# Performance work log

Hardware: AMD Instinct MI355X
Metric: run time of the kernel (lower is better)

The kernel has to match this reference:

```python
import jax, jax.numpy as jnp
import numpy as np

N, E, D_IN, H, Z = 50000, 800000, 256, 96, 32
NEG_SLOPE = 0.2  # PyG GATConv default
BN_EPS = 1e-5


def _gat(x, src, dst, W, a, b, n):
    """Single-head GATConv (PyG semantics, self-loops already in src/dst)."""
    h = x @ W                                   # [N, F']
    e = jax.nn.leaky_relu((h @ a[0])[src] + (h @ a[1])[dst], NEG_SLOPE)  # [E]
    m = jax.ops.segment_max(e, dst, num_segments=n)
    ex = jnp.exp(e - m[dst])
    s = jax.ops.segment_sum(ex, dst, num_segments=n)
    alpha = ex / s[dst]                         # softmax over incoming edges
    out = jax.ops.segment_sum(alpha[:, None] * h[src], dst, num_segments=n)
    return out + b


def _bn(x, g, b):
    # BatchNorm1d in training mode: biased batch stats over nodes
    mu = jnp.mean(x, axis=0)
    v = jnp.var(x, axis=0)
    return g * (x - mu) / jnp.sqrt(v + BN_EPS) + b


def setup_inputs() -> dict:
    key = jax.random.key(0)
    ks = jax.random.split(key, 32)
    inp = {}
    inp["x"] = jax.random.normal(ks[0], (N, D_IN), jnp.float32)
    inp["edge_index"] = jax.random.randint(ks[1], (2, E), 0, N)
    inp["eps"] = jax.random.normal(ks[2], (N, Z), jnp.float32)

    def xav(k, di, do):
        s = float(np.sqrt(2.0 / (di + do)))
        return jax.random.normal(k, (di, do), jnp.float32) * s

    layers = [("enc1", D_IN, H), ("enc2", H, H), ("mu", H, Z), ("lv", H, Z),
              ("dec1", Z, H), ("dec2", H, H), ("out", H, D_IN)]
    ki = 3
    for nm, di, do in layers:
        inp[nm + "_W"] = xav(ks[ki], di, do)
        inp[nm + "_a"] = jax.random.normal(ks[ki + 1], (2, do), jnp.float32) * 0.1
        inp[nm + "_b"] = jnp.zeros((do,), jnp.float32)
        ki += 2
    for nm in ["bne1", "bne2", "bnd1", "bnd2"]:
        inp[nm + "_g"] = jnp.ones((H,), jnp.float32)
        inp[nm + "_b"] = jnp.zeros((H,), jnp.float32)
    return inp


def reference(x, edge_index, eps,
              enc1_W, enc1_a, enc1_b, enc2_W, enc2_a, enc2_b,
              mu_W, mu_a, mu_b, lv_W, lv_a, lv_b,
              dec1_W, dec1_a, dec1_b, dec2_W, dec2_a, dec2_b,
              out_W, out_a, out_b,
              bne1_g, bne1_b, bne2_g, bne2_b, bnd1_g, bnd1_b, bnd2_g, bnd2_b):
    n = x.shape[0]
    loop = jnp.arange(n)
    src = jnp.concatenate([edge_index[0], loop])  # add self-loops (GAT default)
    dst = jnp.concatenate([edge_index[1], loop])

    # ---- GraphEncoder ----
    h0 = jax.nn.relu(_bn(_gat(x, src, dst, enc1_W, enc1_a, enc1_b, n), bne1_g, bne1_b))
    h1 = jax.nn.relu(_bn(_gat(h0, src, dst, enc2_W, enc2_a, enc2_b, n), bne2_g, bne2_b))
    h = h1 + h0  # residual from layer 0
    q_m = _gat(h, src, dst, mu_W, mu_a, mu_b, n)
    q_s = _gat(h, src, dst, lv_W, lv_a, lv_b, n)
    std = jax.nn.softplus(q_s) + 1e-6
    q_z = q_m + std * eps  # rsample

    # ---- GraphDecoder ----
    d0 = jax.nn.relu(_bn(_gat(q_z, src, dst, dec1_W, dec1_a, dec1_b, n), bnd1_g, bnd1_b))
    d1 = jax.nn.relu(_bn(_gat(d0, src, dst, dec2_W, dec2_a, dec2_b, n), bnd2_g, bnd2_b))
    d = d1 + d0
    recon = jax.nn.softmax(_gat(d, src, dst, out_W, out_a, out_b, n), axis=-1)
    return q_z, q_m, q_s, recon
```

## Files before the change

### kernel.cpp

```cpp
#include <hip/hip_runtime.h>
#include <math.h>

#define NN 50000
#define EE 800000
#define HDIM 96
#define ZDIM 32
#define MAXD 64
#define NBUK 64
#define BCAP 16384
#define BMUL 1341
#define NBB 512
#define MGRID 782
#define CDIV(a,b) (((a)+(b)-1)/(b))

typedef unsigned int uint;
typedef unsigned short ushort;
typedef __bf16 bf16x8 __attribute__((ext_vector_type(8)));
typedef float f32x4 __attribute__((ext_vector_type(4)));

__device__ __forceinline__ ushort f2b(float f) {
  uint x = __float_as_uint(f);
  return (ushort)((x + 0x7fffu + ((x >> 16) & 1u)) >> 16);
}
__device__ __forceinline__ uint pack2(float a, float b) {
  return (uint)f2b(a) | ((uint)f2b(b) << 16);
}
__device__ __forceinline__ float blo(uint u) { return __uint_as_float(u << 16); }
__device__ __forceinline__ float bhi(uint u) { return __uint_as_float(u & 0xffff0000u); }
__device__ __forceinline__ float lrelu(float v) { return v > 0.f ? v : 0.2f * v; }

__device__ __forceinline__ void red_scsh(const float* __restrict__ sb,
                                         const float* __restrict__ g,
                                         const float* __restrict__ b,
                                         float* s_c, float* s_h, int tid) {
  if (tid < 96) {
    float su = 0.f, sq = 0.f;
#pragma unroll 8
    for (int j = 0; j < NBUK; j++) {
      su += sb[j * 192 + tid];
      sq += sb[j * 192 + 96 + tid];
    }
    float mu = su * (1.0f / NN);
    float va = sq * (1.0f / NN) - mu * mu;
    float sc = g[tid] * rsqrtf(va + 1e-5f);
    s_c[tid] = sc;
    s_h[tid] = fmaf(-sc, mu, b[tid]);
  }
}

struct PrepArgs { const float* W[7]; const float* a[7]; };

__global__ void k_prep(PrepArgs p, ushort* __restrict__ wt, float* __restrict__ avb,
                       int* __restrict__ zbase, int zcount) {
  const int SDin[6]  = {256, 96, 96, 32, 96, 96};
  const int SDout[6] = {96, 96, 64, 96, 96, 256};
  const int SL[6]    = {0, 1, 2, 4, 5, 6};
  const int SWoff[6] = {0, 24576, 33792, 39936, 43008, 52224};
  int y = blockIdx.y;
  if (y < 6) {
    int Din = SDin[y], Dout = SDout[y];
    int n = Din * Dout;
    ushort* wo = wt + SWoff[y];
    if (y == 2) {
      const float* W2 = p.W[2];
      const float* W3 = p.W[3];
      for (int o = blockIdx.x * 256 + threadIdx.x; o < n; o += 96 * 256) {
        int c = o / Din, k = o % Din;
        float w = (c < 32) ? W2[(size_t)k * 32 + c] : W3[(size_t)k * 32 + (c - 32)];
        wo[o] = f2b(w);
      }
    } else {
      const float* W = p.W[SL[y]];
      for (int o = blockIdx.x * 256 + threadIdx.x; o < n; o += 96 * 256) {
        int c = o / Din, k = o % Din;
        wo[o] = f2b(W[(size_t)k * Dout + c]);
      }
    }
  } else if (y == 6) {
    int wave = (blockIdx.x * 256 + threadIdx.x) >> 6;
    int lane = threadIdx.x & 63;
    for (int row = wave; row < 128; row += 96 * 4) {
      int l = (row < 32) ? 4 : 6;
      int k = (row < 32) ? row : row - 32;
      int Dout = (l == 4) ? 96 : 256;
      const float* W = p.W[l];
      const float* a = p.a[l];
      float s0 = 0.f, s1 = 0.f;
      for (int c = lane; c < Dout; c += 64) {
        float w = W[(size_t)k * Dout + c];
        s0 = fmaf(w, a[c], s0);
        s1 = fmaf(w, a[Dout + c], s1);
      }
      for (int o = 32; o > 0; o >>= 1) {
        s0 += __shfl_down(s0, o);
        s1 += __shfl_down(s1, o);
      }
      if (lane == 0) {
        if (l == 4) { avb[k] = s0; avb[32 + k] = s1; }
        else { avb[64 + k] = s0; avb[160 + k] = s1; }
      }
    }
  } else {
    for (int i = blockIdx.x * 256 + threadIdx.x; i < zcount; i += 96 * 256)
      zbase[i] = 0;
  }
}

__global__ __launch_bounds__(256) void k_partA(const int* __restrict__ eidx,
                                               int* __restrict__ bcnt,
                                               uint* __restrict__ barr) {
  __shared__ int hist[NBUK];
  __shared__ int hbase[NBUK];
  const int tot = EE + NN;
  const int tid = threadIdx.x;
  int base = blockIdx.x * 512 + tid;
  if (tid < NBUK) hist[tid] = 0;
  __syncthreads();
  int dv[2], sv[2], bk[2], ofs[2];
  bool ok[2];
#pragma unroll
  for (int j = 0; j < 2; j++) {
    int e = base + j * 256;
    ok[j] = e < tot;
    dv[j] = sv[j] = bk[j] = ofs[j] = 0;
    if (ok[j]) {
      if (e < EE) { sv[j] = eidx[e]; dv[j] = eidx[EE + e]; }
      else { sv[j] = dv[j] = e - EE; }
      bk[j] = (dv[j] * BMUL) >> 20;
      ofs[j] = atomicAdd(&hist[bk[j]], 1);
    }
  }
  __syncthreads();
  if (tid < NBUK) hbase[tid] = atomicAdd(&bcnt[tid], hist[tid]);
  __syncthreads();
#pragma unroll
  for (int j = 0; j < 2; j++) {
    if (ok[j]) {
      int w = hbase[bk[j]] + ofs[j];
      if (w < BCAP) barr[bk[j] * BCAP + w] = ((uint)dv[j] << 16) | (uint)sv[j];
    }
  }
}

template<int DIN, int DOUT, int AMODE, bool BF16_OUT, bool ADD_BIAS, int EPI, bool STATS>
__device__ __forceinline__ void mfma_body(
    int bid, const void* __restrict__ A1, const void* __restrict__ A2,
    const float* __restrict__ sbA, const float* __restrict__ gA, const float* __restrict__ bA,
    const float* __restrict__ sbB, const float* __restrict__ gB, const float* __restrict__ bB,
    const ushort* __restrict__ Wt, const float* __restrict__ bias,
    void* __restrict__ outp, const float* __restrict__ aA, const float* __restrict__ aB,
    float* __restrict__ el, float* __restrict__ er,
    float2* __restrict__ elp, float2* __restrict__ erp, float* __restrict__ sbout) {
  constexpr int NT = DOUT / 16;
  constexpr int KS = DIN / 32;
  const int tid = threadIdx.x;
  const int lane = tid & 63;
  const int wv = tid >> 6;
  const int row0 = bid * 64 + wv * 16;
  const int cl = lane & 15;
  const int g = lane >> 4;
  const int arow = min(row0 + cl, NN - 1);
  __shared__ float s_c1[96], s_h1[96], s_c2[96], s_h2[96];
  if constexpr (AMODE >= 2) {
    red_scsh(sbA, gA, bA, s_c1, s_h1, tid);
    if constexpr (AMODE == 3) red_scsh(sbB, gB, bB, s_c2, s_h2, tid);
    __syncthreads();
  }
  f32x4 acc[NT];
#pragma unroll
  for (int t = 0; t < NT; t++) acc[t] = (f32x4){0.f, 0.f, 0.f, 0.f};
#pragma unroll
  for (int ks = 0; ks < KS; ks++) {
    bf16x8 af;
    if constexpr (AMODE == 0) {
      af = *(const bf16x8*)((const ushort*)A1 + (size_t)arow * DIN + ks * 32 + g * 8);
    } else if constexpr (AMODE == 1) {
      const float* Af = (const float*)A1 + (size_t)arow * DIN + ks * 32 + g * 8;
      float4 lo = *(const float4*)Af;
      float4 hi = *(const float4*)(Af + 4);
      union { uint4 u; bf16x8 v; } cvt;
      cvt.u.x = pack2(lo.x, lo.y); cvt.u.y = pack2(lo.z, lo.w);
      cvt.u.z = pack2(hi.x, hi.y); cvt.u.w = pack2(hi.z, hi.w);
      af = cvt.v;
    } else {
      const float* p1 = (const float*)A1 + (size_t)arow * DIN + ks * 32 + g * 8;
      const float* p2 = (const float*)A2 + (size_t)arow * DIN + ks * 32 + g * 8;
      const int f0 = ks * 32 + g * 8;
      float v[8];
#pragma unroll
      for (int j = 0; j < 8; j++) {
        float t = fmaxf(fmaf(s_c1[f0 + j], p1[j], s_h1[f0 + j]), 0.f);
        if constexpr (AMODE == 3)
          t += fmaxf(fmaf(s_c2[f0 + j], p2[j], s_h2[f0 + j]), 0.f);
        v[j] = t;
      }
      union { uint4 u; bf16x8 b8; } cv;
      cv.u.x = pack2(v[0], v[1]); cv.u.y = pack2(v[2], v[3]);
      cv.u.z = pack2(v[4], v[5]); cv.u.w = pack2(v[6], v[7]);
      af = cv.b8;
    }
#pragma unroll
    for (int t = 0; t < NT; t++) {
      bf16x8 bf = *(const bf16x8*)(Wt + (size_t)(t * 16 + cl) * DIN + ks * 32 + g * 8);
      acc[t] = __builtin_amdgcn_mfma_f32_16x16x32_bf16(af, bf, acc[t], 0, 0, 0);
    }
  }
  if constexpr (EPI == 1) {
#pragma unroll
    for (int r = 0; r < 4; r++) {
      float l0 = 0.f, l1 = 0.f;
#pragma unroll
      for (int t = 0; t < NT; t++) {
        float w0 = aA[t * 16 + cl], w1 = aA[DOUT + t * 16 + cl];
        l0 = fmaf(acc[t][r], w0, l0);
        l1 = fmaf(acc[t][r], w1, l1);
      }
#pragma unroll
      for (int m = 1; m < 16; m <<= 1) {
        l0 += __shfl_xor(l0, m);
        l1 += __shfl_xor(l1, m);
      }
      int row = row0 + g * 4 + r;
      if (cl == 0 && row < NN) { el[row] = l0; er[row] = l1; }
    }
  }
  if constexpr (EPI == 2) {
#pragma unroll
    for (int r = 0; r < 4; r++) {
      float m0 = 0.f, m1 = 0.f, v0 = 0.f, v1 = 0.f;
#pragma unroll
      for (int t = 0; t < 2; t++) {
        int c = t * 16 + cl;
        m0 = fmaf(acc[t][r], aA[c], m0);
        m1 = fmaf(acc[t][r], aA[32 + c], m1);
        v0 = fmaf(acc[t + 2][r], aB[c], v0);
        v1 = fmaf(acc[t + 2][r], aB[32 + c], v1);
      }
#pragma unroll
      for (int m = 1; m < 16; m <<= 1) {
        m0 += __shfl_xor(m0, m); m1 += __shfl_xor(m1, m);
        v0 += __shfl_xor(v0, m); v1 += __shfl_xor(v1, m);
      }
      int row = row0 + g * 4 + r;
      if (cl == 0 && row < NN) {
        elp[row] = make_float2(m0, v0);
        erp[row] = make_float2(m1, v1);
      }
    }
  }
  if constexpr (ADD_BIAS) {
#pragma unroll
    for (int t = 0; t < NT; t++) {
      float bv = bias[t * 16 + cl];
#pragma unroll
      for (int r = 0; r < 4; r++) acc[t][r] += bv;
    }
  }
  if constexpr (STATS) {
    __shared__ float s_su[96], s_sq[96];
    if (tid < 96) { s_su[tid] = 0.f; s_sq[tid] = 0.f; }
    __syncthreads();
#pragma unroll
    for (int t = 0; t < NT; t++) {
      float su = 0.f, sq = 0.f;
#pragma unroll
      for (int r = 0; r < 4; r++) {
        if (row0 + g * 4 + r < NN) {
          float v = acc[t][r];
          su += v;
          sq = fmaf(v, v, sq);
        }
      }
      atomicAdd(&s_su[t * 16 + cl], su);
      atomicAdd(&s_sq[t * 16 + cl], sq);
    }
    __syncthreads();
    if (tid < 96) {
      float* bk = sbout + (bid & 63) * 192;
      atomicAdd(&bk[tid], s_su[tid]);
      atomicAdd(&bk[96 + tid], s_sq[tid]);
    }
  }
  if constexpr (EPI == 3) {
    float mx[4], sm[4];
#pragma unroll
    for (int r = 0; r < 4; r++) mx[r] = -3.4e38f;
#pragma unroll
    for (int t = 0; t < NT; t++)
#pragma unroll
      for (int r = 0; r < 4; r++) mx[r] = fmaxf(mx[r], acc[t][r]);
#pragma unroll
    for (int r = 0; r < 4; r++) {
#pragma unroll
      for (int msk = 1; msk < 16; msk <<= 1)
        mx[r] = fmaxf(mx[r], __shfl_xor(mx[r], msk));
      sm[r] = 0.f;
    }
#pragma unroll
    for (int t = 0; t < NT; t++)
#pragma unroll
      for (int r = 0; r < 4; r++) { acc[t][r] = expf(acc[t][r] - mx[r]); sm[r] += acc[t][r]; }
#pragma unroll
    for (int r = 0; r < 4; r++) {
#pragma unroll
      for (int msk = 1; msk < 16; msk <<= 1) sm[r] += __shfl_xor(sm[r], msk);
      sm[r] = 1.f / sm[r];
    }
#pragma unroll
    for (int t = 0; t < NT; t++)
#pragma unroll
      for (int r = 0; r < 4; r++) acc[t][r] *= sm[r];
  }
#pragma unroll
  for (int r = 0; r < 4; r++) {
    int grow = row0 + g * 4 + r;
    if (grow >= NN) continue;
    if constexpr (BF16_OUT) {
      ushort* o = (ushort*)outp + (size_t)grow * DOUT + cl;
#pragma unroll
      for (int t = 0; t < NT; t++) o[t * 16] = f2b(acc[t][r]);
    } else {
      float* o = (float*)outp + (size_t)grow * DOUT + cl;
#pragma unroll
      for (int t = 0; t < NT; t++) o[t * 16] = acc[t][r];
    }
  }
}

template<int DIN, int DOUT, int AMODE, bool BF16_OUT, bool ADD_BIAS, int EPI, bool STATS>
__global__ __launch_bounds__(256) void k_mfma(
    const void* __restrict__ A1, const void* __restrict__ A2,
    const float* __restrict__ sbA, const float* __restrict__ gA, const float* __restrict__ bA,
    const float* __restrict__ sbB, const float* __restrict__ gB, const float* __restrict__ bB,
    const ushort* __restrict__ Wt, const float* __restrict__ bias,
    void* __restrict__ outp, const float* __restrict__ aA, const float* __restrict__ aB,
    float* __restrict__ el, float* __restrict__ er,
    float2* __restrict__ elp, float2* __restrict__ erp, float* __restrict__ sbout) {
  mfma_body<DIN, DOUT, AMODE, BF16_OUT, ADD_BIAS, EPI, STATS>(
      blockIdx.x, A1, A2, sbA, gA, bA, sbB, gB, bB, Wt, bias, outp, aA, aB,
      el, er, elp, erp, sbout);
}

__global__ __launch_bounds__(256) void k_fatB(
    const int* __restrict__ bcnt, const uint* __restrict__ barr,
    int* __restrict__ dcnt, ushort* __restrict__ srcs,
    const float* __restrict__ x, const ushort* __restrict__ Wt,
    ushort* __restrict__ hbf, const float* __restrict__ aA,
    float* __restrict__ el, float* __restrict__ er) {
  if (blockIdx.x < NBB) {
    const int bucket = blockIdx.x & 63;
    const int j = blockIdx.x >> 6;
    const int n = min(bcnt[bucket], BCAP);
    const uint* bp = barr + bucket * BCAP;
    for (int idx = j * 256 + (int)threadIdx.x; idx < n; idx += 2048) {
      uint e = bp[idx];
      int d = (int)(e >> 16);
      int s = (int)(e & 0xffffu);
      int p = atomicAdd(&dcnt[d], 1);
      if (p < MAXD) srcs[d * MAXD + p] = (ushort)s;
    }
  } else {
    mfma_body<256, 96, 1, true, false, 1, false>(
        blockIdx.x - NBB, x, nullptr, nullptr, nullptr, nullptr, nullptr, nullptr, nullptr,
        Wt, nullptr, hbf, aA, nullptr, el, er, nullptr, nullptr, nullptr);
  }
}

template<int D, bool BF16O, bool STATS>
__global__ __launch_bounds__(256) void k_agg1(
    const ushort* __restrict__ hb, const float* __restrict__ el,
    const float* __restrict__ er, const int* __restrict__ dcnt,
    const ushort* __restrict__ srcs, const float* __restrict__ bias,
    void* __restrict__ out, float* __restrict__ sbuck) {
  constexpr int LPN = (D <= 32) ? 32 : 64;
  constexpr int NPB = 256 / LPN;
  constexpr int NU = D / 2;
  const int tid = threadIdx.x;
  const int slot = tid / LPN;
  const int ln = tid % LPN;
  const int i = blockIdx.x * NPB + slot;
  const int beg = i * MAXD;
  const int deg = min(dcnt[i], MAXD);
  const int end = beg + deg;
  const float eri = er[i];
  const uint* h32 = (const uint*)hb;
  __shared__ float s_al[256];
  __shared__ uint s_of[256];
  float v0 = -3.4e38f;
  int sv0 = 0;
  if (ln < deg) { sv0 = srcs[beg + ln]; v0 = lrelu(el[sv0] + eri); }
  float m = v0;
  for (int c = beg + LPN; c < end; c += LPN) {
    int e = c + ln;
    if (e < end) m = fmaxf(m, lrelu(el[srcs[e]] + eri));
  }
  for (int o = LPN / 2; o; o >>= 1) m = fmaxf(m, __shfl_xor(m, o, LPN));
  float s = (ln < deg) ? expf(v0 - m) : 0.f;
  for (int c = beg + LPN; c < end; c += LPN) {
    int e = c + ln;
    if (e < end) s += expf(lrelu(el[srcs[e]] + eri) - m);
  }
  for (int o = LPN / 2; o; o >>= 1) s += __shfl_xor(s, o, LPN);
  const float inv = 1.0f / s;
  float acc0 = 0.f, acc1 = 0.f;
  if (ln < deg) { s_al[tid] = expf(v0 - m) * inv; s_of[tid] = (uint)sv0 * NU; }
  const int base = slot * LPN;
  int nv = min(LPN, deg);
  if (ln < NU) {
    int t = 0;
    for (; t + 8 <= nv; t += 8) {
      uint o0 = s_of[base + t],     o1 = s_of[base + t + 1];
      uint o2 = s_of[base + t + 2], o3 = s_of[base + t + 3];
      uint o4 = s_of[base + t + 4], o5 = s_of[base + t + 5];
      uint o6 = s_of[base + t + 6], o7 = s_of[base + t + 7];
      uint u0 = h32[o0 + ln], u1 = h32[o1 + ln], u2 = h32[o2 + ln], u3 = h32[o3 + ln];
      uint u4 = h32[o4 + ln], u5 = h32[o5 + ln], u6 = h32[o6 + ln], u7 = h32[o7 + ln];
      float a0 = s_al[base + t],     a1 = s_al[base + t + 1];
      float a2 = s_al[base + t + 2], a3 = s_al[base + t + 3];
      float a4 = s_al[base + t + 4], a5 = s_al[base + t + 5];
      float a6 = s_al[base + t + 6], a7 = s_al[base + t + 7];
      acc0 = fmaf(a0, blo(u0), acc0); acc1 = fmaf(a0, bhi(u0), acc1);
      acc0 = fmaf(a1, blo(u1), acc0); acc1 = fmaf(a1, bhi(u1), acc1);
      acc0 = fmaf(a2, blo(u2), acc0); acc1 = fmaf(a2, bhi(u2), acc1);
      acc0 = fmaf(a3, blo(u3), acc0); acc1 = fmaf(a3, bhi(u3), acc1);
      acc0 = fmaf(a4, blo(u4), acc0); acc1 = fmaf(a4, bhi(u4), acc1);
      acc0 = fmaf(a5, blo(u5), acc0); acc1 = fmaf(a5, bhi(u5), acc1);
      acc0 = fmaf(a6, blo(u6), acc0); acc1 = fmaf(a6, bhi(u6), acc1);
      acc0 = fmaf(a7, blo(u7), acc0); acc1 = fmaf(a7, bhi(u7), acc1);
    }
    for (; t + 4 <= nv; t += 4) {
      uint o0 = s_of[base + t],     o1 = s_of[base + t + 1];
      uint o2 = s_of[base + t + 2], o3 = s_of[base + t + 3];
      uint u0 = h32[o0 + ln], u1 = h32[o1 + ln], u2 = h32[o2 + ln], u3 = h32[o3 + ln];
      float a0 = s_al[base + t],     a1 = s_al[base + t + 1];
      float a2 = s_al[base + t + 2], a3 = s_al[base + t + 3];
      acc0 = fmaf(a0, blo(u0), acc0); acc1 = fmaf(a0, bhi(u0), acc1);
      acc0 = fmaf(a1, blo(u1), acc0); acc1 = fmaf(a1, bhi(u1), acc1);
      acc0 = fmaf(a2, blo(u2), acc0); acc1 = fmaf(a2, bhi(u2), acc1);
      acc0 = fmaf(a3, blo(u3), acc0); acc1 = fmaf(a3, bhi(u3), acc1);
    }
    for (; t < nv; t++) {
      float a = s_al[base + t];
      uint u = h32[s_of[base + t] + ln];
      acc0 = fmaf(a, blo(u), acc0);
      acc1 = fmaf(a, bhi(u), acc1);
    }
  }
  for (int c = beg + LPN; c < end; c += LPN) {
    int e = c + ln;
    if (e < end) {
      int sv = srcs[e];
      s_al[tid] = expf(lrelu(el[sv] + eri) - m) * inv;
      s_of[tid] = (uint)sv * NU;
    }
    int nv2 = min(LPN, end - c);
    if (ln < NU) {
      for (int t = 0; t < nv2; t++) {
        float a = s_al[base + t];
        uint u = h32[s_of[base + t] + ln];
        acc0 = fmaf(a, blo(u), acc0);
        acc1 = fmaf(a, bhi(u), acc1);
      }
    }
  }
  float o0 = 0.f, o1 = 0.f;
  if (ln < NU) {
    float b0 = bias ? bias[2 * ln] : 0.f;
    float b1 = bias ? bias[2 * ln + 1] : 0.f;
    o0 = acc0 + b0;
    o1 = acc1 + b1;
    if constexpr (BF16O) {
      ((uint*)out)[(size_t)i * NU + ln] = pack2(o0, o1);
    } else {
      ((float2*)out)[(size_t)i * NU + ln] = make_float2(o0, o1);
    }
  }
  if constexpr (STATS) {
    __shared__ float s_val[4][96];
    if (ln < NU) {
      s_val[slot][2 * ln] = o0;
      s_val[slot][2 * ln + 1] = o1;
    }
    __syncthreads();
    if (tid < 96) {
      float su = 0.f, sq = 0.f;
#pragma unroll
      for (int s2 = 0; s2 < 4; s2++) {
        float v = s_val[s2][tid];
        su += v;
        sq = fmaf(v, v, sq);
      }
      float* bk = sbuck + (blockIdx.x & 63) * 192;
      atomicAdd(&bk[tid], su);
      atomicAdd(&bk[96 + tid], sq);
    }
  }
}

__global__ __launch_bounds__(256) void k_aggmulv(
    const ushort* __restrict__ hb, const float2* __restrict__ elp,
    const float2* __restrict__ erp, const int* __restrict__ dcnt,
    const ushort* __restrict__ srcs, const float* __restrict__ bmu,
    const float* __restrict__ blv, float* __restrict__ qm, float* __restrict__ qs,
    const float* __restrict__ eps, float* __restrict__ qz,
    ushort* __restrict__ qzbf, const float* __restrict__ av4,
    float* __restrict__ el, float* __restrict__ er) {
  const int tid = threadIdx.x;
  const int slot = tid >> 5;
  const int ln = tid & 31;
  const int i = blockIdx.x * 8 + slot;
  if (i >= NN) return;
  const int beg = i * MAXD;
  const int deg = min(dcnt[i], MAXD);
  const int end = beg + deg;
  const float2 eri = erp[i];
  const uint* h32 = (const uint*)hb;
  __shared__ float s_am[256];
  __shared__ float s_av[256];
  __shared__ uint s_of[256];
  float v0m = -3.4e38f, v0l = -3.4e38f;
  int sv0 = 0;
  if (ln < deg) {
    sv0 = srcs[beg + ln];
    float2 p = elp[sv0];
    v0m = lrelu(p.x + eri.x);
    v0l = lrelu(p.y + eri.y);
  }
  float mm = v0m, ml = v0l;
  for (int c = beg + 32; c < end; c += 32) {
    int e = c + ln;
    if (e < end) {
      float2 p = elp[srcs[e]];
      mm = fmaxf(mm, lrelu(p.x + eri.x));
      ml = fmaxf(ml, lrelu(p.y + eri.y));
    }
  }
  for (int o = 16; o; o >>= 1) {
    mm = fmaxf(mm, __shfl_xor(mm, o, 32));
    ml = fmaxf(ml, __shfl_xor(ml, o, 32));
  }
  float sm = 0.f, sl = 0.f;
  if (ln < deg) { sm = expf(v0m - mm); sl = expf(v0l - ml); }
  for (int c = beg + 32; c < end; c += 32) {
    int e = c + ln;
    if (e < end) {
      float2 p = elp[srcs[e]];
      sm += expf(lrelu(p.x + eri.x) - mm);
      sl += expf(lrelu(p.y + eri.y) - ml);
    }
  }
  for (int o = 16; o; o >>= 1) {
    sm += __shfl_xor(sm, o, 32);
    sl += __shfl_xor(sl, o, 32);
  }
  const float invm = 1.0f / sm, invl = 1.0f / sl;
  float acc0 = 0.f, acc1 = 0.f;
  if (ln < deg) {
    s_am[tid] = expf(v0m - mm) * invm;
    s_av[tid] = expf(v0l - ml) * invl;
    s_of[tid] = (uint)sv0 * 32;
  }
  const int base = slot * 32;
  const float* s_sel = (ln < 16) ? s_am : s_av;
  int nv = min(32, deg);
  int t = 0;
  for (; t + 4 <= nv; t += 4) {
    uint o0 = s_of[base + t],     o1 = s_of[base + t + 1];
    uint o2 = s_of[base + t + 2], o3 = s_of[base + t + 3];
    uint u0 = h32[o0 + ln], u1 = h32[o1 + ln], u2 = h32[o2 + ln], u3 = h32[o3 + ln];
    float a0 = s_sel[base + t],     a1 = s_sel[base + t + 1];
    float a2 = s_sel[base + t + 2], a3 = s_sel[base + t + 3];
    acc0 = fmaf(a0, blo(u0), acc0); acc1 = fmaf(a0, bhi(u0), acc1);
    acc0 = fmaf(a1, blo(u1), acc0); acc1 = fmaf(a1, bhi(u1), acc1);
    acc0 = fmaf(a2, blo(u2), acc0); acc1 = fmaf(a2, bhi(u2), acc1);
    acc0 = fmaf(a3, blo(u3), acc0); acc1 = fmaf(a3, bhi(u3), acc1);
  }
  for (; t < nv; t++) {
    float a = s_sel[base + t];
    uint u = h32[s_of[base + t] + ln];
    acc0 = fmaf(a, blo(u), acc0);
    acc1 = fmaf(a, bhi(u), acc1);
  }
  for (int c = beg + 32; c < end; c += 32) {
    int e = c + ln;
    if (e < end) {
      int sv = srcs[e];
      float2 p = elp[sv];
      s_am[tid] = expf(lrelu(p.x + eri.x) - mm) * invm;
      s_av[tid] = expf(lrelu(p.y + eri.y) - ml) * invl;
      s_of[tid] = (uint)sv * 32;
    }
    int nv2 = min(32, end - c);
    for (int tt = 0; tt < nv2; tt++) {
      float a = s_sel[base + tt];
      uint u = h32[s_of[base + tt] + ln];
      acc0 = fmaf(a, blo(u), acc0);
      acc1 = fmaf(a, bhi(u), acc1);
    }
  }
  float b0 = (ln < 16) ? bmu[2 * ln] : blv[2 * (ln - 16)];
  float b1 = (ln < 16) ? bmu[2 * ln + 1] : blv[2 * (ln - 16) + 1];
  float o0 = acc0 + b0, o1 = acc1 + b1;
  if (ln < 16) ((float2*)qm)[(size_t)i * 16 + ln] = make_float2(o0, o1);
  else ((float2*)qs)[(size_t)i * 16 + (ln - 16)] = make_float2(o0, o1);
  float q0 = __shfl_xor(o0, 16, 32);
  float q1 = __shfl_xor(o1, 16, 32);
  if (ln < 16) {
    float2 ep = ((const float2*)eps)[(size_t)i * 16 + ln];
    float sp0 = fmaxf(q0, 0.f) + log1pf(expf(-fabsf(q0))) + 1e-6f;
    float sp1 = fmaxf(q1, 0.f) + log1pf(expf(-fabsf(q1))) + 1e-6f;
    float z0 = fmaf(sp0, ep.x, o0);
    float z1 = fmaf(sp1, ep.y, o1);
    ((float2*)qz)[(size_t)i * 16 + ln] = make_float2(z0, z1);
    ((uint*)qzbf)[(size_t)i * 16 + ln] = pack2(z0, z1);
    float d0 = z0 * av4[2 * ln] + z1 * av4[2 * ln + 1];
    float d1 = z0 * av4[32 + 2 * ln] + z1 * av4[32 + 2 * ln + 1];
    for (int o = 8; o; o >>= 1) {
      d0 += __shfl_xor(d0, o, 16);
      d1 += __shfl_xor(d1, o, 16);
    }
    if (ln == 0) { el[i] = d0; er[i] = d1; }
  }
}

__global__ __launch_bounds__(256) void k_bn_dual(
    const float* __restrict__ xA, const float* __restrict__ sbA,
    const float* __restrict__ gA, const float* __restrict__ bA,
    const float* __restrict__ xB, const float* __restrict__ sbB,
    const float* __restrict__ gB, const float* __restrict__ bB,
    ushort* __restrict__ outbf, const float* __restrict__ av, const float* __restrict__ bv,
    float* __restrict__ el, float* __restrict__ er) {
  __shared__ float cA[96], hA[96], cB[96], hB[96];
  const int tid = threadIdx.x;
  red_scsh(sbA, gA, bA, cA, hA, tid);
  red_scsh(sbB, gB, bB, cB, hB, tid);
  __syncthreads();
  const int wv = tid >> 6;
  const int ln = tid & 63;
  for (int it = 0; it < 16; it++) {
    int w = blockIdx.x * 64 + it * 4 + wv;
    if (w >= NN) return;
    const size_t base = (size_t)w * HDIM;
    float v1 = fmaxf(fmaf(cA[ln], xA[base + ln], hA[ln]), 0.f) +
               fmaxf(fmaf(cB[ln], xB[base + ln], hB[ln]), 0.f);
    float v2 = 0.f;
    if (ln < 32) {
      int f = 64 + ln;
      v2 = fmaxf(fmaf(cA[f], xA[base + f], hA[f]), 0.f) +
           fmaxf(fmaf(cB[f], xB[base + f], hB[f]), 0.f);
    }
    outbf[base + ln] = f2b(v1);
    if (ln < 32) outbf[base + 64 + ln] = f2b(v2);
    float d0 = v1 * av[ln], d1 = v1 * bv[ln];
    if (ln < 32) { d0 = fmaf(v2, av[64 + ln], d0); d1 = fmaf(v2, bv[64 + ln], d1); }
    for (int o = 32; o > 0; o >>= 1) {
      d0 += __shfl_down(d0, o);
      d1 += __shfl_down(d1, o);
    }
    if (ln == 0) { el[w] = d0; er[w] = d1; }
  }
}

extern "C" void kernel_launch(void* const* d_in, const int* in_sizes, int n_in,
                              void* d_out, int out_size, void* d_ws, size_t ws_size,
                              hipStream_t stream) {
  const float* x    = (const float*)d_in[0];
  const int*   eidx = (const int*)d_in[1];
  const float* eps  = (const float*)d_in[2];
  const float *W[7], *Aa[7], *Bb[7];
  for (int l = 0; l < 7; l++) {
    W[l]  = (const float*)d_in[3 + 3 * l];
    Aa[l] = (const float*)d_in[4 + 3 * l];
    Bb[l] = (const float*)d_in[5 + 3 * l];
  }
  const float* bng[4] = {(const float*)d_in[24], (const float*)d_in[26],
                         (const float*)d_in[28], (const float*)d_in[30]};
  const float* bnb[4] = {(const float*)d_in[25], (const float*)d_in[27],
                         (const float*)d_in[29], (const float*)d_in[31]};

  size_t off_b = 0;
  auto alloc = [&](size_t bytes) -> void* {
    void* p = (char*)d_ws + off_b;
    off_b = (off_b + bytes + 255) & ~(size_t)255;
    return p;
  };
  ushort* hbf   = (ushort*)alloc((size_t)NN * HDIM * 2);
  ushort* sh2   = (ushort*)alloc((size_t)NN * HDIM * 2);
  float* bufB   = (float*)alloc((size_t)NN * HDIM * 4);
  float* bufD   = (float*)alloc((size_t)NN * HDIM * 4);
  ushort* qzbf  = (ushort*)alloc((size_t)NN * ZDIM * 2);
  float* el     = (float*)alloc((size_t)NN * 4);
  float* er     = (float*)alloc((size_t)NN * 4);
  float2* elp   = (float2*)alloc((size_t)NN * 8);
  float2* erp   = (float2*)alloc((size_t)NN * 8);
  const int ZCNT = NN + NBUK + 4 * NBUK * 192;
  char* zregion = (char*)alloc((size_t)ZCNT * 4);
  int* dcnt     = (int*)zregion;
  int* bcnt     = dcnt + NN;
  float* sb0    = (float*)(bcnt + NBUK);
  float* sb1    = sb0 + NBUK * 192;
  float* sb2    = sb1 + NBUK * 192;
  float* sb3    = sb2 + NBUK * 192;
  ushort* srcs  = (ushort*)alloc((size_t)NN * MAXD * 2);
  uint* barr    = (uint*)alloc((size_t)NBUK * BCAP * 4);
  ushort* wt    = (ushort*)alloc((size_t)76800 * 2);
  float* avb    = (float*)alloc((size_t)256 * 4);
  (void)alloc(65536);

  float* qz    = (float*)d_out;
  float* qm    = qz + (size_t)NN * ZDIM;
  float* qs    = qm + (size_t)NN * ZDIM;
  float* recon = qs + (size_t)NN * ZDIM;

  const int SW[6] = {0, 24576, 33792, 39936, 43008, 52224};
  const float* nf = nullptr;

  PrepArgs pa;
  for (int l = 0; l < 7; l++) { pa.W[l] = W[l]; pa.a[l] = Aa[l]; }
  k_prep<<<dim3(96, 8), 256, 0, stream>>>(pa, wt, avb, dcnt, ZCNT);

  k_partA<<<CDIV(EE + NN, 512), 256, 0, stream>>>(eidx, bcnt, barr);
  k_fatB<<<NBB + MGRID, 256, 0, stream>>>(bcnt, barr, dcnt, srcs,
                                          x, wt + SW[0], hbf, Aa[0], el, er);

  k_agg1<96, false, true><<<CDIV(NN, 4), 256, 0, stream>>>(hbf, el, er, dcnt, srcs,
                                                           Bb[0], bufB, sb0);
  k_mfma<96, 96, 2, true, false, 1, false><<<MGRID, 256, 0, stream>>>(
      bufB, nullptr, sb0, bng[0], bnb[0], nf, nf, nf, wt + SW[1], nullptr, hbf,
      Aa[1], nullptr, el, er, nullptr, nullptr, nullptr);
  k_agg1<96, false, true><<<CDIV(NN, 4), 256, 0, stream>>>(hbf, el, er, dcnt, srcs,
                                                           Bb[1], bufD, sb1);
  k_mfma<96, 64, 3, true, false, 2, false><<<MGRID, 256, 0, stream>>>(
      bufD, bufB, sb1, bng[1], bnb[1], sb0, bng[0], bnb[0], wt + SW[2], nullptr, hbf,
      Aa[2], Aa[3], nullptr, nullptr, elp, erp, nullptr);
  k_aggmulv<<<CDIV(NN, 8), 256, 0, stream>>>(hbf, elp, erp, dcnt, srcs, Bb[2], Bb[3],
                                             qm, qs, eps, qz, qzbf, avb, el, er);

  k_agg1<32, true, false><<<CDIV(NN, 8), 256, 0, stream>>>(qzbf, el, er, dcnt, srcs,
                                                           nullptr, hbf, nullptr);
  k_mfma<32, 96, 0, false, true, 0, true><<<MGRID, 256, 0, stream>>>(
      hbf, nullptr, nf, nf, nf, nf, nf, nf, wt + SW[3], Bb[4], bufB,
      nullptr, nullptr, nullptr, nullptr, nullptr, nullptr, sb2);
  k_mfma<96, 96, 2, true, false, 1, false><<<MGRID, 256, 0, stream>>>(
      bufB, nullptr, sb2, bng[2], bnb[2], nf, nf, nf, wt + SW[4], nullptr, hbf,
      Aa[5], nullptr, el, er, nullptr, nullptr, nullptr);
  k_agg1<96, false, true><<<CDIV(NN, 4), 256, 0, stream>>>(hbf, el, er, dcnt, srcs,
                                                           Bb[5], bufD, sb3);
  k_bn_dual<<<MGRID, 256, 0, stream>>>(bufD, sb3, bng[3], bnb[3],
                                       bufB, sb2, bng[2], bnb[2],
                                       sh2, avb + 64, avb + 160, el, er);
  k_agg1<96, true, false><<<CDIV(NN, 4), 256, 0, stream>>>(sh2, el, er, dcnt, srcs,
                                                           nullptr, hbf, nullptr);
  k_mfma<96, 256, 0, false, true, 3, false><<<MGRID, 256, 0, stream>>>(
      hbf, nullptr, nf, nf, nf, nf, nf, nf, wt + SW[5], Bb[6], recon,
      nullptr, nullptr, nullptr, nullptr, nullptr, nullptr, nullptr);
}
```

Before: 405.9 us.

## Build per-node CSR counts with LDS histograms per bucket, batch partitioning

The CSR fill phase now uses one block per destination bucket. Each block counts per-node degrees in a shared-memory histogram instead of doing global atomics on dcnt, then writes the counts out directly, so dcnt no longer needs zeroing. The partition kernel handles 8 edges per thread instead of 2, which cuts the block count and the global atomics on bucket counts. The trade-off is less parallelism in the fill phase (64 blocks instead of 512); this is partly hidden because those blocks run alongside the GEMM blocks.

```diff
diff --git a/kernel.cpp b/kernel.cpp
--- a/kernel.cpp
+++ b/kernel.cpp
@@ -9,7 +9,7 @@
 #define NBUK 64
 #define BCAP 16384
 #define BMUL 1341
-#define NBB 512
+#define NBB 64
 #define MGRID 782
 #define CDIV(a,b) (((a)+(b)-1)/(b))
 
@@ -28,6 +28,7 @@
 __device__ __forceinline__ float blo(uint u) { return __uint_as_float(u << 16); }
 __device__ __forceinline__ float bhi(uint u) { return __uint_as_float(u & 0xffff0000u); }
 __device__ __forceinline__ float lrelu(float v) { return v > 0.f ? v : 0.2f * v; }
+__device__ __forceinline__ int bukd0(int b) { return (b * 1048576 + 1340) / 1341; }
 
 __device__ __forceinline__ void red_scsh(const float* __restrict__ sb,
                                          const float* __restrict__ g,
@@ -113,13 +114,13 @@
   __shared__ int hbase[NBUK];
   const int tot = EE + NN;
   const int tid = threadIdx.x;
-  int base = blockIdx.x * 512 + tid;
+  int base = blockIdx.x * 2048 + tid;
   if (tid < NBUK) hist[tid] = 0;
   __syncthreads();
-  int dv[2], sv[2], bk[2], ofs[2];
-  bool ok[2];
-#pragma unroll
-  for (int j = 0; j < 2; j++) {
+  int dv[8], sv[8], bk[8], ofs[8];
+  bool ok[8];
+#pragma unroll
+  for (int j = 0; j < 8; j++) {
     int e = base + j * 256;
     ok[j] = e < tot;
     dv[j] = sv[j] = bk[j] = ofs[j] = 0;
@@ -134,7 +135,7 @@
   if (tid < NBUK) hbase[tid] = atomicAdd(&bcnt[tid], hist[tid]);
   __syncthreads();
 #pragma unroll
-  for (int j = 0; j < 2; j++) {
+  for (int j = 0; j < 8; j++) {
     if (ok[j]) {
       int w = hbase[bk[j]] + ofs[j];
       if (w < BCAP) barr[bk[j] * BCAP + w] = ((uint)dv[j] << 16) | (uint)sv[j];
@@ -348,17 +349,36 @@
     ushort* __restrict__ hbf, const float* __restrict__ aA,
     float* __restrict__ el, float* __restrict__ er) {
   if (blockIdx.x < NBB) {
-    const int bucket = blockIdx.x & 63;
-    const int j = blockIdx.x >> 6;
-    const int n = min(bcnt[bucket], BCAP);
-    const uint* bp = barr + bucket * BCAP;
-    for (int idx = j * 256 + (int)threadIdx.x; idx < n; idx += 2048) {
+    const int b = blockIdx.x;
+    const int tid = threadIdx.x;
+    const int d0 = bukd0(b);
+    const int d1 = min(bukd0(b + 1), NN);
+    const int width = d1 - d0;
+    __shared__ int hist[784];
+    for (int t = tid; t < width; t += 256) hist[t] = 0;
+    __syncthreads();
+    const int n = min(bcnt[b], BCAP);
+    const uint* bp = barr + b * BCAP;
+    int idx = tid;
+    for (; idx + 768 < n; idx += 1024) {
+      uint e0 = bp[idx], e1 = bp[idx + 256], e2 = bp[idx + 512], e3 = bp[idx + 768];
+      int p0 = atomicAdd(&hist[(int)(e0 >> 16) - d0], 1);
+      int p1 = atomicAdd(&hist[(int)(e1 >> 16) - d0], 1);
+      int p2 = atomicAdd(&hist[(int)(e2 >> 16) - d0], 1);
+      int p3 = atomicAdd(&hist[(int)(e3 >> 16) - d0], 1);
+      if (p0 < MAXD) srcs[(int)(e0 >> 16) * MAXD + p0] = (ushort)(e0 & 0xffffu);
+      if (p1 < MAXD) srcs[(int)(e1 >> 16) * MAXD + p1] = (ushort)(e1 & 0xffffu);
+      if (p2 < MAXD) srcs[(int)(e2 >> 16) * MAXD + p2] = (ushort)(e2 & 0xffffu);
+      if (p3 < MAXD) srcs[(int)(e3 >> 16) * MAXD + p3] = (ushort)(e3 & 0xffffu);
+    }
+    for (; idx < n; idx += 256) {
       uint e = bp[idx];
       int d = (int)(e >> 16);
-      int s = (int)(e & 0xffffu);
-      int p = atomicAdd(&dcnt[d], 1);
-      if (p < MAXD) srcs[d * MAXD + p] = (ushort)s;
-    }
+      int p = atomicAdd(&hist[d - d0], 1);
+      if (p < MAXD) srcs[d * MAXD + p] = (ushort)(e & 0xffffu);
+    }
+    __syncthreads();
+    for (int t = tid; t < width; t += 256) dcnt[d0 + t] = hist[t];
   } else {
     mfma_body<256, 96, 1, true, false, 1, false>(
         blockIdx.x - NBB, x, nullptr, nullptr, nullptr, nullptr, nullptr, nullptr, nullptr,
@@ -693,10 +713,10 @@
   float* er     = (float*)alloc((size_t)NN * 4);
   float2* elp   = (float2*)alloc((size_t)NN * 8);
   float2* erp   = (float2*)alloc((size_t)NN * 8);
-  const int ZCNT = NN + NBUK + 4 * NBUK * 192;
+  int* dcnt     = (int*)alloc((size_t)NN * 4);
+  const int ZCNT = NBUK + 4 * NBUK * 192;
   char* zregion = (char*)alloc((size_t)ZCNT * 4);
-  int* dcnt     = (int*)zregion;
-  int* bcnt     = dcnt + NN;
+  int* bcnt     = (int*)zregion;
   float* sb0    = (float*)(bcnt + NBUK);
   float* sb1    = sb0 + NBUK * 192;
   float* sb2    = sb1 + NBUK * 192;
@@ -717,9 +737,9 @@
 
   PrepArgs pa;
   for (int l = 0; l < 7; l++) { pa.W[l] = W[l]; pa.a[l] = Aa[l]; }
-  k_prep<<<dim3(96, 8), 256, 0, stream>>>(pa, wt, avb, dcnt, ZCNT);
-
-  k_partA<<<CDIV(EE + NN, 512), 256, 0, stream>>>(eidx, bcnt, barr);
+  k_prep<<<dim3(96, 8), 256, 0, stream>>>(pa, wt, avb, bcnt, ZCNT);
+
+  k_partA<<<CDIV(EE + NN, 2048), 256, 0, stream>>>(eidx, bcnt, barr);
   k_fatB<<<NBB + MGRID, 256, 0, stream>>>(bcnt, barr, dcnt, srcs,
                                           x, wt + SW[0], hbf, Aa[0], el, er);
 
```

After: 375.1 us. 7.6% less time.
